# Kernel optimization log

Hardware: AMD Instinct MI355X
Metric: run time of the kernel (lower is better)

The kernel has to match this reference:

```python
import jax, jax.numpy as jnp
import numpy as np

V, C, L, D = 16384, 16, 6, 64  # n_vars, max_clauses, max_variables, embedding_dim


def _normalize(x):
    # utils.normalize: L2-normalize along the feature axis
    return x / jnp.linalg.norm(x, axis=-1, keepdims=True)


def _rescombine(x, W1, b1, W2, b2):
    # ResidualCombine: normalize(sigmoid(layer1(x)) + layer2(x))
    h = jax.nn.sigmoid(x @ W1 + b1) + x @ W2 + b2
    return _normalize(h)


def setup_inputs() -> dict:
    key = jax.random.key(0)
    ks = jax.random.split(key, 14)
    s = 0.05
    variables = jax.random.normal(ks[0], (V, D), jnp.float32)
    # literal variable indices; slot 0 of every clause is the owning variable i
    lits = jax.random.randint(ks[1], (V, C, L), 0, V)
    lits = lits.at[:, :, 0].set(jnp.arange(V)[:, None])
    neg_mask = jax.random.bernoulli(ks[2], 0.5, (V, C, L))
    # literal validity: at least 2 literals per clause, slot 0 always valid
    nvar = jax.random.randint(ks[3], (V, C), 2, L + 1)
    var_valid = jnp.arange(L)[None, None, :] < nvar[:, :, None]
    # clause validity: at least 1 clause per variable
    nclause = jax.random.randint(ks[4], (V,), 1, C + 1)
    clause_valid = jnp.arange(C)[None, :] < nclause[:, None]
    # params
    Wn = jax.random.normal(ks[5], (D, D), jnp.float32) * s
    bn = jnp.zeros((D,), jnp.float32)
    f = jax.random.normal(ks[6], (D,), jnp.float32)
    false_emb = f / jnp.linalg.norm(f)  # Embedding(1, D, max_norm=1.0)
    W1v = jax.random.normal(ks[7], (L * D, D), jnp.float32) * s
    b1v = jnp.zeros((D,), jnp.float32)
    W2v = jax.random.normal(ks[8], (L * D, D), jnp.float32) * s
    b2v = jnp.zeros((D,), jnp.float32)
    W1c = jax.random.normal(ks[9], (C * D, D), jnp.float32) * s
    b1c = jnp.zeros((D,), jnp.float32)
    W2c = jax.random.normal(ks[10], (C * D, D), jnp.float32) * s
    b2c = jnp.zeros((D,), jnp.float32)
    return dict(variables=variables, lits=lits, neg_mask=neg_mask, var_valid=var_valid,
                clause_valid=clause_valid, Wn=Wn, bn=bn, false_emb=false_emb,
                W1v=W1v, b1v=b1v, W2v=W2v, b2v=b2v, W1c=W1c, b1c=b1c, W2c=W2c, b2c=b2c)


def reference(variables, lits, neg_mask, var_valid, clause_valid,
              Wn, bn, false_emb, W1v, b1v, W2v, b2v, W1c, b1c, W2c, b2c):
    # gather literal embeddings: [V, C, L, D]
    g = variables[lits]
    # negation linear for negative literals
    v = jnp.where(neg_mask[..., None], g @ Wn + bn, g)
    # pad invalid literal slots with the 'false' embedding
    v = jnp.where(var_valid[..., None], v, false_emb)
    # variable_combiner over flattened [L*D]
    clause_emb = _rescombine(v.reshape(V, C, L * D), W1v, b1v, W2v, b2v)  # [V, C, D]
    # pad missing clauses with 'true' = negation(false)
    true_emb = false_emb @ Wn + bn
    clause_emb = jnp.where(clause_valid[..., None], clause_emb, true_emb)
    # clause_combiner over flattened [C*D]
    out = _rescombine(clause_emb.reshape(V, C * D), W1c, b1c, W2c, b2c)  # [V, D]
    # variables with no clauses pass through unchanged
    has_clauses = clause_valid.any(axis=-1)
    return jnp.where(has_clauses[:, None], out, variables)
```

## Files before the change

### kernel.cpp

```cpp
#include <hip/hip_runtime.h>
#include <hip/hip_bf16.h>

#define NV 16384
#define NC 16
#define NL 6
#define ND 64

typedef unsigned short u16;
typedef unsigned int u32;
typedef __attribute__((ext_vector_type(8))) short short8;
typedef __attribute__((ext_vector_type(4))) unsigned short u16x4;
typedef __attribute__((ext_vector_type(4))) int i32x4;
typedef __attribute__((ext_vector_type(4))) float f32x4;

#define PB_BN  0
#define PB_FE  64
#define PB_B1V 128
#define PB_B2V 192
#define PB_B1C 256
#define PB_B2C 320
#define U_BVS   896
#define U_BCS   50048
#define U_BN    181120
#define U_VARSB 185216
#define U_NEGB  1233856
#define U_FIDX  2282496

__device__ __forceinline__ float ldbf(const u16* p, int i) {
  return __uint_as_float(((u32)p[i]) << 16);
}
__device__ __forceinline__ u16 f2b(float f) {
  u32 x = __float_as_uint(f);
  return (u16)((x + 0x7FFF + ((x >> 16) & 1)) >> 16);
}
__device__ __forceinline__ int ldmask(const void* p, int i, int bdt) {
  return bdt ? (int)((const signed char*)p)[i] : ((const int*)p)[i];
}
__device__ __forceinline__ int ldmask_nt(const void* p, int i, int bdt) {
  return bdt ? (int)__builtin_nontemporal_load((const signed char*)p + i)
             : __builtin_nontemporal_load((const int*)p + i);
}
__device__ __forceinline__ float ldf(const void* p, int i, int fdt) {
  return fdt ? ldbf((const u16*)p, i) : ((const float*)p)[i];
}
__device__ __forceinline__ void gll16(const u16* g, u16* l) {
  __builtin_amdgcn_global_load_lds(
      (const __attribute__((address_space(1))) u32*)(g),
      (__attribute__((address_space(3))) u32*)(l), 16, 0, 0);
}

__global__ __launch_bounds__(256) void k_prep(
    const void* vars, const int* __restrict__ lits, const void* negm, const void* vval,
    const void* Wn, const void* bn, const void* femb,
    const void* W1v, const void* b1v, const void* W2v, const void* b2v,
    const void* W1c, const void* b1c, const void* W2c, const void* b2c,
    int* flags, float* pbuf, u16* wsB) {
  __shared__ int s_cnt[4], s_big[4];
  __shared__ u16 wn[64 * 72];
  const int t = threadIdx.x;
  {
    const u32 w = ((const u32*)vars)[t];
    const u32 e = (w >> 7) & 0xFF;
    const unsigned long long bal = __ballot(e >= 0x6E && e <= 0x8E);
    const u32 bw = ((const u32*)vval)[t];
    const unsigned long long bb = __ballot(bw > 1u);
    if ((t & 63) == 0) { s_cnt[t >> 6] = __popcll(bal); s_big[t >> 6] = (bb != 0ull); }
  }
  __syncthreads();
  const int fdt = (s_cnt[0] + s_cnt[1] + s_cnt[2] + s_cnt[3]) >= 192;
  const int bdt = (s_big[0] | s_big[1] | s_big[2] | s_big[3]);
  const int bid = blockIdx.x;

  if (bid == 0) {
    if (t == 0) { flags[0] = fdt; flags[1] = bdt; }
    if (t < 64) {
      const void* src[6] = {bn, femb, b1v, b2v, b1c, b2c};
      const int off[6] = {PB_BN, PB_FE, PB_B1V, PB_B2V, PB_B1C, PB_B2C};
      for (int j = 0; j < 6; j++) pbuf[off[j] + t] = ldf(src[j], t, fdt);
      wsB[U_VARSB + NV * 64 + t] = fdt ? ((const u16*)femb)[t] : f2b(((const float*)femb)[t]);
    }
  } else if (bid < 25) {
    const int c = (bid - 1) * 256 + t;
    const int ln = c & 63, nt = (c >> 6) & 7, ks = c >> 9;
    const int n = nt * 16 + (ln & 15);
    const void* src = (n < 64) ? W1v : W2v;
    const int kb = ks * 32 + (ln >> 4) * 8, n6 = n & 63;
    u16 o[8];
#pragma unroll
    for (int j = 0; j < 8; j++) o[j] = f2b(ldf(src, (kb + j) * 64 + n6, fdt));
    *(short8*)(wsB + U_BVS + c * 8) = *(short8*)o;
  } else if (bid < 89) {
    const int c = (bid - 25) * 256 + t;
    const int ln = c & 63, nt = (c >> 6) & 7, ks = c >> 9;
    const int n = nt * 16 + (ln & 15);
    const void* src = (n < 64) ? W1c : W2c;
    const int kb = ks * 32 + (ln >> 4) * 8, n6 = n & 63;
    u16 o[8];
#pragma unroll
    for (int j = 0; j < 8; j++) o[j] = f2b(ldf(src, (kb + j) * 64 + n6, fdt));
    *(short8*)(wsB + U_BCS + c * 8) = *(short8*)o;
  } else if (bid < 601) {
    const int c8 = (bid - 89) * 256 + t;
    u16 o[8];
    if (fdt) {
      *(short8*)o = ((const short8*)vars)[c8];
    } else {
      const float* f = (const float*)vars + c8 * 8;
#pragma unroll
      for (int j = 0; j < 8; j++) o[j] = f2b(f[j]);
    }
    *(short8*)(wsB + U_VARSB + c8 * 8) = *(short8*)o;
  } else if (bid < 1369) {
    const int i0 = ((bid - 601) * 256 + t) * 8;
    const i32x4 l0 = __builtin_nontemporal_load((const i32x4*)((const int*)lits + i0));
    const i32x4 l1 = __builtin_nontemporal_load((const i32x4*)((const int*)lits + i0) + 1);
    int nm[8], vv[8];
    if (bdt) {
      const unsigned long long nmq =
          __builtin_nontemporal_load((const unsigned long long*)((const signed char*)negm + i0));
      const unsigned long long vvq =
          __builtin_nontemporal_load((const unsigned long long*)((const signed char*)vval + i0));
#pragma unroll
      for (int j = 0; j < 8; j++) {
        nm[j] = (int)((nmq >> (8 * j)) & 0xFF);
        vv[j] = (int)((vvq >> (8 * j)) & 0xFF);
      }
    } else {
      const i32x4 n0 = __builtin_nontemporal_load((const i32x4*)((const int*)negm + i0));
      const i32x4 n1 = __builtin_nontemporal_load((const i32x4*)((const int*)negm + i0) + 1);
      const i32x4 v0 = __builtin_nontemporal_load((const i32x4*)((const int*)vval + i0));
      const i32x4 v1 = __builtin_nontemporal_load((const i32x4*)((const int*)vval + i0) + 1);
#pragma unroll
      for (int j = 0; j < 4; j++) {
        nm[j] = n0[j]; nm[4 + j] = n1[j];
        vv[j] = v0[j]; vv[4 + j] = v1[j];
      }
    }
    u16 o[8];
#pragma unroll
    for (int j = 0; j < 8; j++) {
      const int idx = (j < 4) ? l0[j] : l1[j - 4];
      o[j] = (u16)(vv[j] ? (idx + (nm[j] ? (NV + 1) : 0)) : NV);
    }
    __builtin_nontemporal_store(*(short8*)o, (short8*)(wsB + U_FIDX + i0));
  } else {
    const int nb = bid - 1369;
    for (int e = t; e < 4096; e += 256) {
      const int k = e >> 6, n = e & 63;
      wn[n * 72 + k] = f2b(ldf(Wn, e, fdt));
    }
    __syncthreads();
    const int lane = t & 63, wv = t >> 6;
    const int col = lane & 15, quad = lane >> 4, q8 = quad * 8;
    const int rowbase = nb * 64 + wv * 16;
    f32x4 acc[4];
#pragma unroll
    for (int nt = 0; nt < 4; nt++) acc[nt] = (f32x4){0.f, 0.f, 0.f, 0.f};
    const int arow = min(rowbase + col, NV);
#pragma unroll
    for (int ks = 0; ks < 2; ks++) {
      short8 a;
      if (fdt) {
        const u16* ap = (arow == NV) ? (const u16*)femb : (const u16*)vars + arow * 64;
        a = *(const short8*)(ap + ks * 32 + q8);
      } else {
        const float* ap = (arow == NV) ? (const float*)femb : (const float*)vars + arow * 64;
        const f32x4 f0 = *(const f32x4*)(ap + ks * 32 + q8);
        const f32x4 f1 = *(const f32x4*)(ap + ks * 32 + q8 + 4);
#pragma unroll
        for (int j = 0; j < 4; j++) { a[j] = (short)f2b(f0[j]); a[4 + j] = (short)f2b(f1[j]); }
      }
#pragma unroll
      for (int nt = 0; nt < 4; nt++) {
        const short8 b = *(const short8*)(&wn[(nt * 16 + col) * 72 + ks * 32 + q8]);
        acc[nt] = __builtin_amdgcn_mfma_f32_16x16x32_bf16(a, b, acc[nt], 0, 0, 0);
      }
    }
#pragma unroll
    for (int reg = 0; reg < 4; reg++) {
      const int r = rowbase + quad * 4 + reg;
      if (r <= NV) {
#pragma unroll
        for (int nt = 0; nt < 4; nt++) {
          const int d = nt * 16 + col;
          wsB[U_NEGB + r * 64 + d] = f2b(acc[nt][reg] + ldf(bn, d, fdt));
        }
      }
    }
  }
}

__global__ __launch_bounds__(512, 4) void k_main(
    const void* __restrict__ vars, const void* __restrict__ cval,
    const float* __restrict__ pbuf, const int* __restrict__ flags,
    const u16* __restrict__ wsB, void* __restrict__ outv) {
  __shared__ __align__(16) u16 smem[24576];
  __shared__ float ps[16][4];
  __shared__ int hcS[16];

  const int tid = threadIdx.x, lane = tid & 63, wv = tid >> 6;
  const int col = lane & 15, quad = lane >> 4, q8 = quad * 8;
  const int fdt = flags[0], bdt = flags[1];
  const int vbase = blockIdx.x * 16 + wv * 2;
  const int v0 = blockIdx.x * 16;

  u32 r2_[2][3];
#pragma unroll
  for (int v4 = 0; v4 < 2; v4++)
#pragma unroll
    for (int i = 0; i < 3; i++)
      r2_[v4][i] = __builtin_nontemporal_load(
          (const u32*)(wsB + U_FIDX + (vbase + v4) * 96 + col * 6 + i * 2));

  const int cv = ldmask_nt(cval, vbase * 16 + (lane & 31), bdt);
  const unsigned long long bal = __ballot(cv != 0);
  if (lane < 2) hcS[wv * 2 + lane] = ((bal >> (lane * 16)) & 0xFFFFull) != 0;

  f32x4 acc[2][8];
#pragma unroll
  for (int v4 = 0; v4 < 2; v4++)
#pragma unroll
    for (int nt = 0; nt < 8; nt++) acc[v4][nt] = (f32x4){0.f, 0.f, 0.f, 0.f};

#pragma unroll
  for (int j = 0; j < 3; j++) {
    const int cl = wv * 3 + j;
    gll16(wsB + U_BVS + cl * 512 + lane * 8, &smem[cl * 512]);
  }
  short8 a_[3][2];
#pragma unroll
  for (int v4 = 0; v4 < 2; v4++) {
    const int idx = (int)(r2_[v4][0] & 0xFFFFu);
    a_[0][v4] = *(const short8*)(wsB + U_VARSB + idx * 64 + q8);
    a_[1][v4] = *(const short8*)(wsB + U_VARSB + idx * 64 + 32 + q8);
  }
  __syncthreads();

  for (int q = 0; q < 4; q++) {
    if (q < 3) {
#pragma unroll
      for (int j = 0; j < 3; j++) {
        const int cl = wv * 3 + j;
        gll16(wsB + U_BVS + (q + 1) * 12288 + cl * 512 + lane * 8,
              &smem[((q + 1) & 1) * 12288 + cl * 512]);
      }
    }
#pragma unroll
    for (int ksl = 0; ksl < 3; ksl++) {
      const int gk = q * 3 + ksl;
      const int gn = gk + 2;
      const int sf = (ksl + 2) % 3;
      if (gn < 12) {
        const int goff = (gn & 1) * 32 + q8;
        const int pi = gn >> 2, ph = (gn >> 1) & 1;
#pragma unroll
        for (int v4 = 0; v4 < 2; v4++) {
          const int idx = (int)((r2_[v4][pi] >> (ph * 16)) & 0xFFFFu);
          a_[sf][v4] = *(const short8*)(wsB + U_VARSB + idx * 64 + goff);
        }
      }
      __builtin_amdgcn_s_setprio(1);
#pragma unroll
      for (int nt = 0; nt < 8; nt++) {
        const short8 b = *(const short8*)(&smem[(q & 1) * 12288 + (ksl * 8 + nt) * 512 + lane * 8]);
#pragma unroll
        for (int v4 = 0; v4 < 2; v4++)
          acc[v4][nt] = __builtin_amdgcn_mfma_f32_16x16x32_bf16(a_[ksl][v4], b, acc[v4][nt], 0, 0, 0);
      }
      __builtin_amdgcn_s_setprio(0);
    }
    if (q < 3) __syncthreads();
  }
  __syncthreads();

  {
    float b1l[4], b2l[4], truel[4];
#pragma unroll
    for (int nt = 0; nt < 4; nt++) {
      const int d = nt * 16 + col;
      b1l[nt] = pbuf[PB_B1V + d];
      b2l[nt] = pbuf[PB_B2V + d];
      truel[nt] = ldbf(wsB, U_NEGB + NV * 64 + d);
    }
#pragma unroll
    for (int v4 = 0; v4 < 2; v4++) {
      const u32 vmask = (u32)((bal >> (v4 * 16)) & 0xFFFFull);
      const int vloc = wv * 2 + v4;
#pragma unroll
      for (int reg = 0; reg < 4; reg++) {
        const int c = quad * 4 + reg;
        float hh[4], ss = 0.f;
#pragma unroll
        for (int nt = 0; nt < 4; nt++) {
          hh[nt] = 1.0f / (1.0f + __expf(-(acc[v4][nt][reg] + b1l[nt]))) + acc[v4][nt + 4][reg] + b2l[nt];
          ss += hh[nt] * hh[nt];
        }
        ss += __shfl_xor(ss, 1, 64); ss += __shfl_xor(ss, 2, 64);
        ss += __shfl_xor(ss, 4, 64); ss += __shfl_xor(ss, 8, 64);
        const float sc = 1.0f / sqrtf(ss);
        const int valid = (vmask >> c) & 1;
#pragma unroll
        for (int nt = 0; nt < 4; nt++) {
          const float o = valid ? hh[nt] * sc : truel[nt];
          const int l2 = (nt * 2 + (col >> 3)) & 3;
          smem[(c * 2 + (nt >> 1)) * 512 + (l2 * 16 + vloc) * 8 + (col & 7)] = f2b(o);
        }
      }
    }
  }
  __syncthreads();

  const int g = wv & 3, kh = wv >> 2;
  f32x4 acc1 = (f32x4){0.f, 0.f, 0.f, 0.f}, acc2 = (f32x4){0.f, 0.f, 0.f, 0.f};
#pragma unroll 8
  for (int ks = kh * 16; ks < kh * 16 + 16; ks++) {
    const short8 a = *(const short8*)(&smem[ks * 512 + lane * 8]);
    const short8 b1 = *(const short8*)(wsB + U_BCS + (ks * 8 + g) * 512 + lane * 8);
    const short8 b2 = *(const short8*)(wsB + U_BCS + (ks * 8 + g + 4) * 512 + lane * 8);
    acc1 = __builtin_amdgcn_mfma_f32_16x16x32_bf16(a, b1, acc1, 0, 0, 0);
    acc2 = __builtin_amdgcn_mfma_f32_16x16x32_bf16(a, b2, acc2, 0, 0, 0);
  }
  float* red = (float*)(smem + 16384);
  if (kh) {
    const int base = (g * 64 + lane) * 8;
    *(f32x4*)(red + base) = acc1;
    *(f32x4*)(red + base + 4) = acc2;
  }
  __syncthreads();

  float h[4];
  if (!kh) {
    const int base = (g * 64 + lane) * 8;
    acc1 += *(const f32x4*)(red + base);
    acc2 += *(const f32x4*)(red + base + 4);
    const int d = g * 16 + col;
    const float b1c_d = pbuf[PB_B1C + d], b2c_d = pbuf[PB_B2C + d];
#pragma unroll
    for (int reg = 0; reg < 4; reg++) {
      h[reg] = 1.0f / (1.0f + __expf(-(acc1[reg] + b1c_d))) + acc2[reg] + b2c_d;
      float ssp = h[reg] * h[reg];
      ssp += __shfl_xor(ssp, 1, 64); ssp += __shfl_xor(ssp, 2, 64);
      ssp += __shfl_xor(ssp, 4, 64); ssp += __shfl_xor(ssp, 8, 64);
      if (col == 0) ps[quad * 4 + reg][g] = ssp;
    }
  }
  __syncthreads();
  if (!kh) {
    const int d = g * 16 + col;
#pragma unroll
    for (int reg = 0; reg < 4; reg++) {
      const int r = quad * 4 + reg;
      const float tot = ps[r][0] + ps[r][1] + ps[r][2] + ps[r][3];
      float o = h[reg] * (1.0f / sqrtf(tot));
      const int oi = (v0 + r) * 64 + d;
      if (hcS[r]) {
        if (fdt) __builtin_nontemporal_store(f2b(o), &((u16*)outv)[oi]);
        else __builtin_nontemporal_store(o, &((float*)outv)[oi]);
      } else {
        if (fdt) __builtin_nontemporal_store(
            __builtin_nontemporal_load(&((const u16*)vars)[oi]), &((u16*)outv)[oi]);
        else __builtin_nontemporal_store(
            __builtin_nontemporal_load(&((const float*)vars)[oi]), &((float*)outv)[oi]);
      }
    }
  }
}

extern "C" void kernel_launch(void* const* d_in, const int* in_sizes, int n_in,
                              void* d_out, int out_size, void* d_ws, size_t ws_size,
                              hipStream_t stream) {
  const void* vars = d_in[0];
  const int* lits = (const int*)d_in[1];
  const void* negm = d_in[2];
  const void* vval = d_in[3];
  const void* cvalid = d_in[4];
  const void* Wn = d_in[5];
  const void* bn = d_in[6];
  const void* femb = d_in[7];
  const void* W1v = d_in[8];
  const void* b1v = d_in[9];
  const void* W2v = d_in[10];
  const void* b2v = d_in[11];
  const void* W1c = d_in[12];
  const void* b1c = d_in[13];
  const void* W2c = d_in[14];
  const void* b2c = d_in[15];

  int* flags = (int*)d_ws;
  float* pbuf = (float*)((char*)d_ws + 256);
  u16* wsB = (u16*)d_ws;

  k_prep<<<1626, 256, 0, stream>>>(vars, lits, negm, vval, Wn, bn, femb,
                                   W1v, b1v, W2v, b2v, W1c, b1c, W2c, b2c,
                                   flags, pbuf, wsB);
  k_main<<<NV / 16, 512, 0, stream>>>(vars, cvalid, pbuf, flags, wsB, d_out);
}
```

Measured before the change: 152.3 us.

## Fuse literal-index packing into main kernel and bf16 vars copy into negation GEMM

Removes two prep-stage jobs. The packed literal-index buffer is no longer written in prep; k_main now reads lits, neg_mask and var_valid directly and computes the packed indices in registers. The bf16 copy of the variables is now stored by the negation-GEMM blocks, which already load those rows. This drops a full write-then-read round trip of the index array through global memory and shrinks the prep grid. In exchange, k_main reads the wider int32 lits and masks in a less coalesced 6-element-per-lane pattern.

```diff
diff --git a/kernel.cpp b/kernel.cpp
--- a/kernel.cpp
+++ b/kernel.cpp
@@ -10,6 +10,7 @@
 typedef unsigned int u32;
 typedef __attribute__((ext_vector_type(8))) short short8;
 typedef __attribute__((ext_vector_type(4))) unsigned short u16x4;
+typedef __attribute__((ext_vector_type(2))) int i32x2;
 typedef __attribute__((ext_vector_type(4))) int i32x4;
 typedef __attribute__((ext_vector_type(4))) float f32x4;
 
@@ -21,10 +22,8 @@
 #define PB_B2C 320
 #define U_BVS   896
 #define U_BCS   50048
-#define U_BN    181120
 #define U_VARSB 185216
 #define U_NEGB  1233856
-#define U_FIDX  2282496
 
 __device__ __forceinline__ float ldbf(const u16* p, int i) {
   return __uint_as_float(((u32)p[i]) << 16);
@@ -32,9 +31,6 @@
 __device__ __forceinline__ u16 f2b(float f) {
   u32 x = __float_as_uint(f);
   return (u16)((x + 0x7FFF + ((x >> 16) & 1)) >> 16);
-}
-__device__ __forceinline__ int ldmask(const void* p, int i, int bdt) {
-  return bdt ? (int)((const signed char*)p)[i] : ((const int*)p)[i];
 }
 __device__ __forceinline__ int ldmask_nt(const void* p, int i, int bdt) {
   return bdt ? (int)__builtin_nontemporal_load((const signed char*)p + i)
@@ -99,52 +95,8 @@
 #pragma unroll
     for (int j = 0; j < 8; j++) o[j] = f2b(ldf(src, (kb + j) * 64 + n6, fdt));
     *(short8*)(wsB + U_BCS + c * 8) = *(short8*)o;
-  } else if (bid < 601) {
-    const int c8 = (bid - 89) * 256 + t;
-    u16 o[8];
-    if (fdt) {
-      *(short8*)o = ((const short8*)vars)[c8];
-    } else {
-      const float* f = (const float*)vars + c8 * 8;
-#pragma unroll
-      for (int j = 0; j < 8; j++) o[j] = f2b(f[j]);
-    }
-    *(short8*)(wsB + U_VARSB + c8 * 8) = *(short8*)o;
-  } else if (bid < 1369) {
-    const int i0 = ((bid - 601) * 256 + t) * 8;
-    const i32x4 l0 = __builtin_nontemporal_load((const i32x4*)((const int*)lits + i0));
-    const i32x4 l1 = __builtin_nontemporal_load((const i32x4*)((const int*)lits + i0) + 1);
-    int nm[8], vv[8];
-    if (bdt) {
-      const unsigned long long nmq =
-          __builtin_nontemporal_load((const unsigned long long*)((const signed char*)negm + i0));
-      const unsigned long long vvq =
-          __builtin_nontemporal_load((const unsigned long long*)((const signed char*)vval + i0));
-#pragma unroll
-      for (int j = 0; j < 8; j++) {
-        nm[j] = (int)((nmq >> (8 * j)) & 0xFF);
-        vv[j] = (int)((vvq >> (8 * j)) & 0xFF);
-      }
-    } else {
-      const i32x4 n0 = __builtin_nontemporal_load((const i32x4*)((const int*)negm + i0));
-      const i32x4 n1 = __builtin_nontemporal_load((const i32x4*)((const int*)negm + i0) + 1);
-      const i32x4 v0 = __builtin_nontemporal_load((const i32x4*)((const int*)vval + i0));
-      const i32x4 v1 = __builtin_nontemporal_load((const i32x4*)((const int*)vval + i0) + 1);
-#pragma unroll
-      for (int j = 0; j < 4; j++) {
-        nm[j] = n0[j]; nm[4 + j] = n1[j];
-        vv[j] = v0[j]; vv[4 + j] = v1[j];
-      }
-    }
-    u16 o[8];
-#pragma unroll
-    for (int j = 0; j < 8; j++) {
-      const int idx = (j < 4) ? l0[j] : l1[j - 4];
-      o[j] = (u16)(vv[j] ? (idx + (nm[j] ? (NV + 1) : 0)) : NV);
-    }
-    __builtin_nontemporal_store(*(short8*)o, (short8*)(wsB + U_FIDX + i0));
   } else {
-    const int nb = bid - 1369;
+    const int nb = bid - 89;
     for (int e = t; e < 4096; e += 256) {
       const int k = e >> 6, n = e & 63;
       wn[n * 72 + k] = f2b(ldf(Wn, e, fdt));
@@ -170,6 +122,7 @@
 #pragma unroll
         for (int j = 0; j < 4; j++) { a[j] = (short)f2b(f0[j]); a[4 + j] = (short)f2b(f1[j]); }
       }
+      *(short8*)(wsB + U_VARSB + arow * 64 + ks * 32 + q8) = a;
 #pragma unroll
       for (int nt = 0; nt < 4; nt++) {
         const short8 b = *(const short8*)(&wn[(nt * 16 + col) * 72 + ks * 32 + q8]);
@@ -192,6 +145,8 @@
 
 __global__ __launch_bounds__(512, 4) void k_main(
     const void* __restrict__ vars, const void* __restrict__ cval,
+    const int* __restrict__ lits, const void* __restrict__ negm,
+    const void* __restrict__ vval,
     const float* __restrict__ pbuf, const int* __restrict__ flags,
     const u16* __restrict__ wsB, void* __restrict__ outv) {
   __shared__ __align__(16) u16 smem[24576];
@@ -206,11 +161,46 @@
 
   u32 r2_[2][3];
 #pragma unroll
-  for (int v4 = 0; v4 < 2; v4++)
+  for (int v4 = 0; v4 < 2; v4++) {
+    const int vv_ = vbase + v4;
+    const int eo = vv_ * 96 + col * 6;
+    int li[6], nm[6], vv[6];
+    {
+      const i32x2* lp = (const i32x2*)((const int*)lits + eo);
+      const i32x2 a0 = __builtin_nontemporal_load(lp);
+      const i32x2 a1 = __builtin_nontemporal_load(lp + 1);
+      const i32x2 a2 = __builtin_nontemporal_load(lp + 2);
+      li[0] = a0[0]; li[1] = a0[1]; li[2] = a1[0]; li[3] = a1[1]; li[4] = a2[0]; li[5] = a2[1];
+    }
+    if (bdt) {
+      const u16* np = (const u16*)((const signed char*)negm + eo);
+      const u16* vp = (const u16*)((const signed char*)vval + eo);
+#pragma unroll
+      for (int i = 0; i < 3; i++) {
+        const u32 wn_ = __builtin_nontemporal_load(np + i);
+        const u32 wv_ = __builtin_nontemporal_load(vp + i);
+        nm[2 * i] = wn_ & 0xFF; nm[2 * i + 1] = (wn_ >> 8) & 0xFF;
+        vv[2 * i] = wv_ & 0xFF; vv[2 * i + 1] = (wv_ >> 8) & 0xFF;
+      }
+    } else {
+      const i32x2* np = (const i32x2*)((const int*)negm + eo);
+      const i32x2* vp = (const i32x2*)((const int*)vval + eo);
+#pragma unroll
+      for (int i = 0; i < 3; i++) {
+        const i32x2 wn_ = __builtin_nontemporal_load(np + i);
+        const i32x2 wv_ = __builtin_nontemporal_load(vp + i);
+        nm[2 * i] = wn_[0]; nm[2 * i + 1] = wn_[1];
+        vv[2 * i] = wv_[0]; vv[2 * i + 1] = wv_[1];
+      }
+    }
+    u32 fid[6];
+#pragma unroll
+    for (int j = 0; j < 6; j++)
+      fid[j] = vv[j] ? (u32)(li[j] + (nm[j] ? (NV + 1) : 0)) : (u32)NV;
 #pragma unroll
     for (int i = 0; i < 3; i++)
-      r2_[v4][i] = __builtin_nontemporal_load(
-          (const u32*)(wsB + U_FIDX + (vbase + v4) * 96 + col * 6 + i * 2));
+      r2_[v4][i] = fid[2 * i] | (fid[2 * i + 1] << 16);
+  }
 
   const int cv = ldmask_nt(cval, vbase * 16 + (lane & 31), bdt);
   const unsigned long long bal = __ballot(cv != 0);
@@ -390,8 +380,9 @@
   float* pbuf = (float*)((char*)d_ws + 256);
   u16* wsB = (u16*)d_ws;
 
-  k_prep<<<1626, 256, 0, stream>>>(vars, lits, negm, vval, Wn, bn, femb,
-                                   W1v, b1v, W2v, b2v, W1c, b1c, W2c, b2c,
-                                   flags, pbuf, wsB);
-  k_main<<<NV / 16, 512, 0, stream>>>(vars, cvalid, pbuf, flags, wsB, d_out);
-}
+  k_prep<<<346, 256, 0, stream>>>(vars, lits, negm, vval, Wn, bn, femb,
+                                  W1v, b1v, W2v, b2v, W1c, b1c, W2c, b2c,
+                                  flags, pbuf, wsB);
+  k_main<<<NV / 16, 512, 0, stream>>>(vars, cvalid, lits, negm, vval,
+                                      pbuf, flags, wsB, d_out);
+}
```

After: 150.4 us. No clear change (-1.3%).
